# Kernel optimization log

Hardware: AMD Instinct MI355X
Metric: run time of the kernel (lower is better)

The kernel has to match this reference:

```python
import jax, jax.numpy as jnp
import numpy as np
from jax import lax

MIN_R = 0.01
RADIUS = 0.8
NSAMPLE = 32
PRED_NSAMPLE = 16
TEMPERATURE = 1.0
DIV_COEF = 10.0
GRID3 = 64  # grid_size**3, grid_size=4
EPS = 1e-5


def _ball_query(q, xyz, radius, nsample):
    """q (M,3), xyz (N,3), radius scalar or (M,). Returns idx (M,nsample) int32, empty (M,) bool.
    Mirrors stack ball_query CUDA op: first-found neighbors within radius, padded with first index."""
    N = xyz.shape[0]
    d2 = jnp.sum((q[:, None, :] - xyz[None, :, :]) ** 2, axis=-1)  # (M,N)
    r = jnp.broadcast_to(jnp.asarray(radius, d2.dtype), (q.shape[0],))[:, None]
    valid = d2 < r * r
    score = jnp.where(valid, -jnp.arange(N, dtype=jnp.int32), -(N + 1))
    vals, _ = lax.top_k(score, nsample)  # largest score == smallest valid index
    idx = -vals
    pad = idx == (N + 1)
    idx = jnp.where(pad, idx[:, :1], idx)  # pad with first found neighbor
    empty = pad[:, 0]                       # no neighbor at all
    idx = jnp.where(empty[:, None], 0, idx)
    return idx, empty


def _group(q, xyz, feats, idx, empty):
    """QueryAndGroup gather: relative xyz concat point features; zero empty queries.
    Returns (M, nsample, 3+C)."""
    g_xyz = xyz[idx] - q[:, None, :]
    g = jnp.concatenate([g_xyz, feats[idx]], axis=-1)
    return jnp.where(empty[:, None, None], jnp.zeros((), g.dtype), g)


def _mlp(x, params):
    """Shared 1x1 Conv2d + BatchNorm2d(training stats) + ReLU stack. x: (B,M,S,C)."""
    for W, g, b in params:
        x = jnp.einsum('bmsc,cd->bmsd', x, W)
        mu = x.mean(axis=(0, 1, 2))
        var = x.var(axis=(0, 1, 2))
        x = (x - mu) * lax.rsqrt(var + EPS) * g + b
        x = jax.nn.relu(x)
    return x


def setup_inputs() -> dict:
    key = jax.random.key(0)
    ks = jax.random.split(key, 16)
    B, N, C, R, Croi = 2, 8192, 32, 64, 128
    scene = jnp.array([10.0, 10.0, 4.0], jnp.float32)
    xyz = jax.random.uniform(ks[0], (B, N, 3), jnp.float32) * scene
    features = jax.random.normal(ks[1], (B, N, C), jnp.float32)
    rois = jax.random.uniform(ks[2], (B, R, GRID3, 3), jnp.float32) * scene
    roi_features = jax.random.normal(ks[3], (B, R, Croi), jnp.float32)

    def kaiming(k, fi, fo):
        return jax.random.normal(k, (fi, fo), jnp.float32) * np.float32(np.sqrt(2.0 / fi))

    return {
        'xyz': xyz, 'features': features, 'rois': rois, 'roi_features': roi_features,
        'temperature_decay': jnp.ones((1,), jnp.float32),
        # predict mlp: [32+3, 32, 32]
        'pw0': kaiming(ks[4], 35, 32), 'pg0': jnp.ones(32), 'pb0': jnp.zeros(32),
        'pw1': kaiming(ks[5], 32, 32), 'pg1': jnp.ones(32), 'pb1': jnp.zeros(32),
        # feat mlp: [32+3, 64, 64]
        'fw0': kaiming(ks[6], 35, 64), 'fg0': jnp.ones(64), 'fb0': jnp.zeros(64),
        'fw1': kaiming(ks[7], 64, 64), 'fg1': jnp.ones(64), 'fb1': jnp.zeros(64),
        # predict fc: [32*64 + 128, 1]
        'fcw': kaiming(ks[8], 2176, 1), 'fcb': jnp.zeros(1),
    }


def reference(xyz, features, rois, roi_features, temperature_decay,
              pw0, pg0, pb0, pw1, pg1, pb1,
              fw0, fg0, fb0, fw1, fg1, fb1, fcw, fcb):
    B, num_rois = rois.shape[0], rois.shape[1]
    new_xyz = rois.reshape(B, -1, 3)  # (B, M, 3), M = num_rois*grid^3

    # ---- radius-prediction branch: fixed-radius grouping + MLP + max-pool ----
    idx_p, empty_p = jax.vmap(lambda q, x: _ball_query(q, x, RADIUS, PRED_NSAMPLE))(new_xyz, xyz)
    gp = jax.vmap(_group)(new_xyz, xyz, features, idx_p, empty_p)  # (B,M,S,3+C)
    gp = _mlp(gp, [(pw0, pg0, pb0), (pw1, pg1, pb1)])
    pooled = gp.max(axis=2)                       # (B, M, Cp)
    pooled = pooled.reshape(B, num_rois, -1)      # (B, R, grid^3*Cp)
    res = jnp.concatenate([pooled, roi_features], axis=-1) @ fcw + fcb  # (B,R,1)
    r = jnp.maximum(res / DIV_COEF + RADIUS, MIN_R)
    r_pts = jnp.broadcast_to(r, (B, num_rois, GRID3)).reshape(B, -1)    # (B, M)

    # ---- deformable branch: per-query radius grouping + soft weights ----
    idx_d, empty_d = jax.vmap(lambda q, x, rr: _ball_query(q, x, rr, NSAMPLE))(new_xyz, xyz, r_pts)
    gd = jax.vmap(_group)(new_xyz, xyz, features, idx_d, empty_d)       # (B,M,S,3+C)
    dist = jnp.linalg.norm(gd[..., :3], axis=-1)                        # (B,M,S)
    w = jax.nn.sigmoid((r_pts[..., None] - dist) / (TEMPERATURE * temperature_decay[0]))
    w = jnp.where(empty_d[..., None], jnp.zeros((), w.dtype), w)
    gd = _mlp(gd, [(fw0, fg0, fb0), (fw1, fg1, fb1)])                   # (B,M,S,Cout)
    new_feats = (w[..., None] * gd).max(axis=2)                          # (B,M,Cout)

    return new_xyz.reshape(-1, 3), new_feats.reshape(-1, new_feats.shape[-1])
```

## Files before the change

kernel.cpp:

```cpp
#include <hip/hip_runtime.h>

#define NB 2
#define NPTS 8192
#define NQ 4096
#define MTOT 8192
#define SP 16
#define SD 32
#define CIN 32
#define CP 32
#define CF 64
#define NROI 128
#define RADIUS_C 0.8f
#define MIN_R_C 0.01f
#define DIV_COEF_C 10.0f

__device__ int   g_idx_p[MTOT * SP];
__device__ int   g_empty_p[MTOT];
__device__ int   g_idx_d[MTOT * SD];
__device__ int   g_empty_d[MTOT];
__device__ float g_xa[(size_t)MTOT * SD * CF];
__device__ float g_xb[(size_t)MTOT * SD * CF];
__device__ float g_psT[CF * 2048];
__device__ float g_pqT[CF * 2048];
__device__ float g_bnscale[4][CF];
__device__ float g_bnshift[4][CF];
__device__ float g_pdot[MTOT];
__device__ float g_rroi[NROI];

__global__ void copy_xyz_kernel(const float* __restrict__ rois, float* __restrict__ out) {
    int i = blockIdx.x * 256 + threadIdx.x;
    if (i < MTOT * 3) out[i] = rois[i];
}

template <int NS>
__launch_bounds__(256, 8)
__global__ void bq_kernel(const float* __restrict__ xyz, const float* __restrict__ newxyz) {
    int lane = threadIdx.x & 63;
    int q = blockIdx.x * 4 + (threadIdx.x >> 6);
    int b = q >> 12;
    const float* xb = xyz + (size_t)b * NPTS * 3;
    float qx = newxyz[q * 3 + 0], qy = newxyz[q * 3 + 1], qz = newxyz[q * 3 + 2];
    float r = (NS == SP) ? RADIUS_C : g_rroi[q >> 6];
    float r2 = r * r;
    int* idx_out   = (NS == SP) ? g_idx_p   : g_idx_d;
    int* empty_out = (NS == SP) ? g_empty_p : g_empty_d;

    int cnt = 0, first_idx = 0;
    float cx = xb[3 * lane + 0];
    float cy = xb[3 * lane + 1];
    float cz = xb[3 * lane + 2];
    for (int g = 0; g < NPTS / 64 && cnt < NS; ++g) {
        int pn = (((g + 1) & 127) << 6) + lane;
        float nx = xb[3 * pn + 0];
        float ny = xb[3 * pn + 1];
        float nz = xb[3 * pn + 2];
        float dx = qx - cx, dy = qy - cy, dz = qz - cz;
        float d2 = dx * dx + dy * dy + dz * dz;
        bool valid = d2 < r2;
        unsigned long long mask = __ballot(valid);
        if (cnt == 0 && mask) first_idx = (g << 6) + (int)__builtin_ctzll(mask);
        int pos = cnt + __popcll(mask & ((1ull << lane) - 1ull));
        if (valid && pos < NS) idx_out[q * NS + pos] = (g << 6) + lane;
        cnt += __popcll(mask);
        cx = nx; cy = ny; cz = nz;
    }
    if (cnt == 0) {
        if (lane < NS) idx_out[q * NS + lane] = 0;
        if (lane == 0) empty_out[q] = 1;
    } else {
        int filled = cnt < NS ? cnt : NS;
        if (lane >= filled && lane < NS) idx_out[q * NS + lane] = first_idx;
        if (lane == 0) empty_out[q] = 0;
    }
}


template <int NS, int CH>
__launch_bounds__(128, 4)
__global__ void mlp_passA_kernel(const float* __restrict__ xyz, const float* __restrict__ feats,
                                 const float* __restrict__ newxyz, const float* __restrict__ W0,
                                 float* __restrict__ xout) {
    constexpr int GSTR = 37;
    constexpr int SST  = CH + 2;
    __shared__ float buf[128 * GSTR];
    __shared__ float ls[128], lq[128];
    int tid = threadIdx.x;
    int rowbase = blockIdx.x * 128;
    int row = rowbase + tid;
    int q = row / NS, b = q >> 12;
    const int* idx_arr = (NS == SP) ? g_idx_p : g_idx_d;
    const int* emp_arr = (NS == SP) ? g_empty_p : g_empty_d;
    {
        float* dst = &buf[tid * GSTR];
        if (emp_arr[q]) {
#pragma unroll
            for (int c = 0; c < 35; ++c) dst[c] = 0.f;
        } else {
            int idx = idx_arr[row];
            const float* xp = xyz + (size_t)b * NPTS * 3 + idx * 3;
            dst[0] = xp[0] - newxyz[q * 3 + 0];
            dst[1] = xp[1] - newxyz[q * 3 + 1];
            dst[2] = xp[2] - newxyz[q * 3 + 2];
            const float4* fp = (const float4*)(feats + (size_t)b * NPTS * CIN + (size_t)idx * CIN);
#pragma unroll
            for (int j = 0; j < 8; ++j) {
                float4 v = fp[j];
                dst[3 + 4 * j + 0] = v.x; dst[3 + 4 * j + 1] = v.y;
                dst[3 + 4 * j + 2] = v.z; dst[3 + 4 * j + 3] = v.w;
            }
        }
    }
    float acc[CH];
#pragma unroll
    for (int ch = 0; ch < CH; ++ch) acc[ch] = 0.f;
    {
        const float* inrow = &buf[tid * GSTR];
        for (int c = 0; c < 35; ++c) {
            float h = inrow[c];
#pragma unroll
            for (int ch = 0; ch < CH; ++ch) acc[ch] = fmaf(h, W0[c * CH + ch], acc[ch]);
        }
    }
    float sum = 0.f, sq = 0.f;
#pragma unroll
    for (int p = 0; p < 2; ++p) {
        __syncthreads();
        if ((tid >> 6) == p) {
            float* srow = &buf[(tid & 63) * SST];
#pragma unroll
            for (int ch = 0; ch < CH; ++ch) srow[ch] = acc[ch];
        }
        __syncthreads();
        if (CH == 64) {
            int ch = tid & 63, rg = tid >> 6;
            for (int r = 0; r < 32; ++r) {
                float v = buf[(rg * 32 + r) * SST + ch];
                xout[(size_t)(rowbase + p * 64 + rg * 32 + r) * CH + ch] = v;
                sum += v; sq += v * v;
            }
        } else {
            int ch = tid & 31, rg = tid >> 5;
            for (int r = 0; r < 16; ++r) {
                float v = buf[(rg * 16 + r) * SST + ch];
                xout[(size_t)(rowbase + p * 64 + rg * 16 + r) * CH + ch] = v;
                sum += v; sq += v * v;
            }
        }
    }
    ls[tid] = sum; lq[tid] = sq;
    __syncthreads();
    if (CH == 64) {
        if (tid < 64) {
            g_psT[tid * 2048 + blockIdx.x] = ls[tid] + ls[64 + tid];
            g_pqT[tid * 2048 + blockIdx.x] = lq[tid] + lq[64 + tid];
        }
    } else {
        if (tid < 32) {
            g_psT[tid * 2048 + blockIdx.x] = ls[tid] + ls[32 + tid] + ls[64 + tid] + ls[96 + tid];
            g_pqT[tid * 2048 + blockIdx.x] = lq[tid] + lq[32 + tid] + lq[64 + tid] + lq[96 + tid];
        }
    }
}

template <int NS, int CH>
__launch_bounds__(128, 4)
__global__ void mlp_passB_kernel(const float* __restrict__ W1, const float* __restrict__ xin,
                                 float* __restrict__ xout, int bn0) {
    constexpr int HSTR = 33;
    constexpr int SST  = CH + 2;
    __shared__ float buf[128 * 37];
    __shared__ float ls[128], lq[128];
    int tid = threadIdx.x;
    int rowbase = blockIdx.x * 128;
    const float* sc0 = g_bnscale[bn0];
    const float* sh0 = g_bnshift[bn0];
    float acc2[CH];
#pragma unroll
    for (int ch = 0; ch < CH; ++ch) acc2[ch] = 0.f;
    const float4* src = (const float4*)xin;
#pragma unroll
    for (int hc = 0; hc < CH / 32; ++hc) {
        if (hc) __syncthreads();
#pragma unroll
        for (int k = 0; k < 8; ++k) {
            int o4 = tid + k * 128;
            int rloc = o4 >> 3, j = o4 & 7;
            int c = 4 * j, gc = hc * 32 + c;
            float4 v = src[(size_t)(rowbase + rloc) * (CH / 4) + hc * 8 + j];
            float* d = &buf[rloc * HSTR + c];
            d[0] = fmaxf(fmaf(v.x, sc0[gc + 0], sh0[gc + 0]), 0.f);
            d[1] = fmaxf(fmaf(v.y, sc0[gc + 1], sh0[gc + 1]), 0.f);
            d[2] = fmaxf(fmaf(v.z, sc0[gc + 2], sh0[gc + 2]), 0.f);
            d[3] = fmaxf(fmaf(v.w, sc0[gc + 3], sh0[gc + 3]), 0.f);
        }
        __syncthreads();
        const float* hrow = &buf[tid * HSTR];
        for (int c = 0; c < 32; ++c) {
            float h = hrow[c];
#pragma unroll
            for (int ch = 0; ch < CH; ++ch)
                acc2[ch] = fmaf(h, W1[(hc * 32 + c) * CH + ch], acc2[ch]);
        }
    }
    float sum = 0.f, sq = 0.f;
#pragma unroll
    for (int p = 0; p < 2; ++p) {
        __syncthreads();
        if ((tid >> 6) == p) {
            float* srow = &buf[(tid & 63) * SST];
#pragma unroll
            for (int ch = 0; ch < CH; ++ch) srow[ch] = acc2[ch];
        }
        __syncthreads();
        if (CH == 64) {
            int ch = tid & 63, rg = tid >> 6;
            for (int r = 0; r < 32; ++r) {
                float v = buf[(rg * 32 + r) * SST + ch];
                xout[(size_t)(rowbase + p * 64 + rg * 32 + r) * CH + ch] = v;
                sum += v; sq += v * v;
            }
        } else {
            int ch = tid & 31, rg = tid >> 5;
            for (int r = 0; r < 16; ++r) {
                float v = buf[(rg * 16 + r) * SST + ch];
                xout[(size_t)(rowbase + p * 64 + rg * 16 + r) * CH + ch] = v;
                sum += v; sq += v * v;
            }
        }
    }
    ls[tid] = sum; lq[tid] = sq;
    __syncthreads();
    if (CH == 64) {
        if (tid < 64) {
            g_psT[tid * 2048 + blockIdx.x] = ls[tid] + ls[64 + tid];
            g_pqT[tid * 2048 + blockIdx.x] = lq[tid] + lq[64 + tid];
        }
    } else {
        if (tid < 32) {
            g_psT[tid * 2048 + blockIdx.x] = ls[tid] + ls[32 + tid] + ls[64 + tid] + ls[96 + tid];
            g_pqT[tid * 2048 + blockIdx.x] = lq[tid] + lq[32 + tid] + lq[64 + tid] + lq[96 + tid];
        }
    }
}

__global__ void passC_f_kernel(const float* __restrict__ xyz, const float* __restrict__ newxyz,
                               const float* __restrict__ td, const float* __restrict__ xin,
                               float* __restrict__ out) {
    __shared__ float lw[64];
    int tid = threadIdx.x;
    int qpair = blockIdx.x * 2;
    if (tid < 64) {
        int ql = tid >> 5, s = tid & 31;
        int q = qpair + ql;
        float wv = 0.f;
        if (!g_empty_d[q]) {
            int idx = g_idx_d[q * SD + s];
            int b = q >> 12;
            float dx = xyz[(size_t)b * NPTS * 3 + idx * 3 + 0] - newxyz[q * 3 + 0];
            float dy = xyz[(size_t)b * NPTS * 3 + idx * 3 + 1] - newxyz[q * 3 + 1];
            float dz = xyz[(size_t)b * NPTS * 3 + idx * 3 + 2] - newxyz[q * 3 + 2];
            float dist = sqrtf(dx * dx + dy * dy + dz * dz);
            float rq = g_rroi[q >> 6];
            wv = 1.f / (1.f + expf(-(rq - dist) / td[0]));
        }
        lw[tid] = wv;
    }
    __syncthreads();
    int ql = tid >> 6, ch = tid & 63;
    int q = qpair + ql;
    float sc = g_bnscale[3][ch], sh = g_bnshift[3][ch];
    float m = 0.f;
    for (int s = 0; s < SD; ++s) {
        float v = xin[((size_t)q * SD + s) * CF + ch];
        m = fmaxf(m, lw[ql * 32 + s] * fmaxf(fmaf(v, sc, sh), 0.f));
    }
    out[MTOT * 3 + (size_t)q * CF + ch] = m;
}

__global__ void passC_p_kernel(const float* __restrict__ fcw, const float* __restrict__ xin) {
    int tid = threadIdx.x;
    int q = blockIdx.x * 8 + (tid >> 5);
    int ch = tid & 31;
    float sc = g_bnscale[1][ch], sh = g_bnshift[1][ch];
    float m = 0.f;
    for (int s = 0; s < SP; ++s) {
        float v = xin[(size_t)(q * SP + s) * CP + ch] * sc + sh;
        m = fmaxf(m, fmaxf(v, 0.f));
    }
    float pd = m * fcw[(q & 63) * CP + ch];
    for (int off = 16; off > 0; off >>= 1) pd += __shfl_down(pd, off, 32);
    if (ch == 0) g_pdot[q] = pd;
}

__global__ void finalize_kernel(const float* __restrict__ gamma, const float* __restrict__ beta,
                                float n, int layer, int nblocks) {
    __shared__ double l_s[256], l_q[256];
    int ch = blockIdx.x, tid = threadIdx.x;
    double s = 0, q = 0;
    for (int i = tid; i < nblocks; i += 256) { s += g_psT[ch * 2048 + i]; q += g_pqT[ch * 2048 + i]; }
    l_s[tid] = s; l_q[tid] = q; __syncthreads();
    for (int off = 128; off > 0; off >>= 1) {
        if (tid < off) { l_s[tid] += l_s[tid + off]; l_q[tid] += l_q[tid + off]; }
        __syncthreads();
    }
    if (tid == 0) {
        double mu = l_s[0] / (double)n;
        double var = l_q[0] / (double)n - mu * mu;
        if (var < 0) var = 0;
        double sc = (double)gamma[ch] / sqrt(var + 1e-5);
        g_bnscale[layer][ch] = (float)sc;
        g_bnshift[layer][ch] = (float)((double)beta[ch] - mu * sc);
    }
}

__global__ void roi_r_kernel(const float* __restrict__ roif, const float* __restrict__ fcw,
                             const float* __restrict__ fcb) {
    int tid = threadIdx.x;
    int roi = blockIdx.x * 4 + (tid >> 6);
    int lane = tid & 63;
    float acc = g_pdot[roi * 64 + lane]
              + roif[roi * 128 + lane]      * fcw[2048 + lane]
              + roif[roi * 128 + 64 + lane] * fcw[2048 + 64 + lane];
    for (int off = 32; off > 0; off >>= 1) acc += __shfl_down(acc, off, 64);
    if (lane == 0) {
        float res = acc + fcb[0];
        g_rroi[roi] = fmaxf(res / DIV_COEF_C + RADIUS_C, MIN_R_C);
    }
}

extern "C" void kernel_launch(void* const* d_in, const int* in_sizes, int n_in,
                              void* d_out, int out_size, void* d_ws, size_t ws_size,
                              hipStream_t stream) {
    const float* xyz   = (const float*)d_in[0];
    const float* feats = (const float*)d_in[1];
    const float* rois  = (const float*)d_in[2];
    const float* roif  = (const float*)d_in[3];
    const float* td    = (const float*)d_in[4];
    const float* pw0 = (const float*)d_in[5];
    const float* pg0 = (const float*)d_in[6];
    const float* pb0 = (const float*)d_in[7];
    const float* pw1 = (const float*)d_in[8];
    const float* pg1 = (const float*)d_in[9];
    const float* pb1 = (const float*)d_in[10];
    const float* fw0 = (const float*)d_in[11];
    const float* fg0 = (const float*)d_in[12];
    const float* fb0 = (const float*)d_in[13];
    const float* fw1 = (const float*)d_in[14];
    const float* fg1 = (const float*)d_in[15];
    const float* fb1 = (const float*)d_in[16];
    const float* fcw = (const float*)d_in[17];
    const float* fcb = (const float*)d_in[18];
    float* out = (float*)d_out;

    float* xa; hipGetSymbolAddress((void**)&xa, HIP_SYMBOL(g_xa));
    float* xb; hipGetSymbolAddress((void**)&xb, HIP_SYMBOL(g_xb));

    copy_xyz_kernel<<<96, 256, 0, stream>>>(rois, out);

    bq_kernel<SP><<<MTOT / 4, 256, 0, stream>>>(xyz, rois);
    mlp_passA_kernel<SP, CP><<<1024, 128, 0, stream>>>(xyz, feats, rois, pw0, xa);
    finalize_kernel<<<CP, 256, 0, stream>>>(pg0, pb0, (float)(MTOT * SP), 0, 1024);
    mlp_passB_kernel<SP, CP><<<1024, 128, 0, stream>>>(pw1, xa, xb, 0);
    finalize_kernel<<<CP, 256, 0, stream>>>(pg1, pb1, (float)(MTOT * SP), 1, 1024);
    passC_p_kernel<<<MTOT / 8, 256, 0, stream>>>(fcw, xb);
    roi_r_kernel<<<NROI / 4, 256, 0, stream>>>(roif, fcw, fcb);

    bq_kernel<SD><<<MTOT / 4, 256, 0, stream>>>(xyz, rois);
    mlp_passA_kernel<SD, CF><<<2048, 128, 0, stream>>>(xyz, feats, rois, fw0, xa);
    finalize_kernel<<<CF, 256, 0, stream>>>(fg0, fb0, (float)(MTOT * SD), 2, 2048);
    mlp_passB_kernel<SD, CF><<<2048, 128, 0, stream>>>(fw1, xa, xb, 2);
    finalize_kernel<<<CF, 256, 0, stream>>>(fg1, fb1, (float)(MTOT * SD), 3, 2048);
    passC_f_kernel<<<MTOT / 2, 128, 0, stream>>>(xyz, rois, td, xb, out);
}
```

Measured before the change: 309.6 us.

## Store deformable-branch MLP activations in fp16 and tile ball query through LDS

The deformable branch's intermediate activations (8192x32x64) are now stored as fp16 instead of fp32, with a dedicated fp16 second-layer kernel and fp16 reads in the final pooling kernel. This halves the global-memory traffic for the largest buffers. The ball query now loads 512-point tiles into shared memory cooperatively per block and exits early once all waves are full. The costs are reduced precision in the stored pre-BN activations and extra block-level syncs in the ball query.

```diff
diff --git a/kernel.cpp b/kernel.cpp
--- a/kernel.cpp
+++ b/kernel.cpp
@@ -1,4 +1,5 @@
 #include <hip/hip_runtime.h>
+#include <hip/hip_fp16.h>
 
 #define NB 2
 #define NPTS 8192
@@ -13,13 +14,14 @@
 #define RADIUS_C 0.8f
 #define MIN_R_C 0.01f
 #define DIV_COEF_C 10.0f
+#define TILE 512
 
 __device__ int   g_idx_p[MTOT * SP];
 __device__ int   g_empty_p[MTOT];
 __device__ int   g_idx_d[MTOT * SD];
 __device__ int   g_empty_d[MTOT];
-__device__ float g_xa[(size_t)MTOT * SD * CF];
-__device__ float g_xb[(size_t)MTOT * SD * CF];
+__device__ unsigned char g_xa[(size_t)MTOT * SD * CF * 2];
+__device__ unsigned char g_xb[(size_t)MTOT * SD * CF * 2];
 __device__ float g_psT[CF * 2048];
 __device__ float g_pqT[CF * 2048];
 __device__ float g_bnscale[4][CF];
@@ -35,10 +37,14 @@
 template <int NS>
 __launch_bounds__(256, 8)
 __global__ void bq_kernel(const float* __restrict__ xyz, const float* __restrict__ newxyz) {
-    int lane = threadIdx.x & 63;
-    int q = blockIdx.x * 4 + (threadIdx.x >> 6);
+    __shared__ float4 l4[TILE * 3 / 4];
+    __shared__ int s_active;
+    int tid = threadIdx.x;
+    int wave = tid >> 6, lane = tid & 63;
+    int q = blockIdx.x * 4 + wave;
     int b = q >> 12;
-    const float* xb = xyz + (size_t)b * NPTS * 3;
+    const float4* xb4 = (const float4*)(xyz + (size_t)b * NPTS * 3);
+    const float* lp = (const float*)l4;
     float qx = newxyz[q * 3 + 0], qy = newxyz[q * 3 + 1], qz = newxyz[q * 3 + 2];
     float r = (NS == SP) ? RADIUS_C : g_rroi[q >> 6];
     float r2 = r * r;
@@ -46,23 +52,29 @@
     int* empty_out = (NS == SP) ? g_empty_p : g_empty_d;
 
     int cnt = 0, first_idx = 0;
-    float cx = xb[3 * lane + 0];
-    float cy = xb[3 * lane + 1];
-    float cz = xb[3 * lane + 2];
-    for (int g = 0; g < NPTS / 64 && cnt < NS; ++g) {
-        int pn = (((g + 1) & 127) << 6) + lane;
-        float nx = xb[3 * pn + 0];
-        float ny = xb[3 * pn + 1];
-        float nz = xb[3 * pn + 2];
-        float dx = qx - cx, dy = qy - cy, dz = qz - cz;
-        float d2 = dx * dx + dy * dy + dz * dz;
-        bool valid = d2 < r2;
-        unsigned long long mask = __ballot(valid);
-        if (cnt == 0 && mask) first_idx = (g << 6) + (int)__builtin_ctzll(mask);
-        int pos = cnt + __popcll(mask & ((1ull << lane) - 1ull));
-        if (valid && pos < NS) idx_out[q * NS + pos] = (g << 6) + lane;
-        cnt += __popcll(mask);
-        cx = nx; cy = ny; cz = nz;
+    for (int t = 0; t < NPTS / TILE; ++t) {
+        l4[tid] = xb4[t * 384 + tid];
+        if (tid + 256 < 384) l4[tid + 256] = xb4[t * 384 + tid + 256];
+        if (tid == 0) s_active = 0;
+        __syncthreads();
+        if (cnt < NS) {
+            for (int s = 0; s < TILE / 64; ++s) {
+                int pl = s * 64 + lane;
+                float dx = qx - lp[3 * pl + 0];
+                float dy = qy - lp[3 * pl + 1];
+                float dz = qz - lp[3 * pl + 2];
+                bool valid = (dx * dx + dy * dy + dz * dz) < r2;
+                unsigned long long mask = __ballot(valid);
+                if (cnt == 0 && mask) first_idx = t * TILE + s * 64 + (int)__builtin_ctzll(mask);
+                int pos = cnt + __popcll(mask & ((1ull << lane) - 1ull));
+                if (valid && pos < NS) idx_out[q * NS + pos] = t * TILE + s * 64 + lane;
+                cnt += __popcll(mask);
+                if (cnt >= NS) break;
+            }
+            if (cnt < NS && lane == 0) s_active = 1;
+        }
+        __syncthreads();
+        if (!s_active) break;
     }
     if (cnt == 0) {
         if (lane < NS) idx_out[q * NS + lane] = 0;
@@ -74,12 +86,11 @@
     }
 }
 
-
-template <int NS, int CH>
+template <int NS, int CH, bool HALF>
 __launch_bounds__(128, 4)
 __global__ void mlp_passA_kernel(const float* __restrict__ xyz, const float* __restrict__ feats,
                                  const float* __restrict__ newxyz, const float* __restrict__ W0,
-                                 float* __restrict__ xout) {
+                                 void* __restrict__ xout_) {
     constexpr int GSTR = 37;
     constexpr int SST  = CH + 2;
     __shared__ float buf[128 * GSTR];
@@ -121,6 +132,8 @@
             for (int ch = 0; ch < CH; ++ch) acc[ch] = fmaf(h, W0[c * CH + ch], acc[ch]);
         }
     }
+    float* xf = (float*)xout_;
+    __half* xh = (__half*)xout_;
     float sum = 0.f, sq = 0.f;
 #pragma unroll
     for (int p = 0; p < 2; ++p) {
@@ -135,14 +148,16 @@
             int ch = tid & 63, rg = tid >> 6;
             for (int r = 0; r < 32; ++r) {
                 float v = buf[(rg * 32 + r) * SST + ch];
-                xout[(size_t)(rowbase + p * 64 + rg * 32 + r) * CH + ch] = v;
+                size_t o = (size_t)(rowbase + p * 64 + rg * 32 + r) * CH + ch;
+                if (HALF) xh[o] = __float2half_rn(v); else xf[o] = v;
                 sum += v; sq += v * v;
             }
         } else {
             int ch = tid & 31, rg = tid >> 5;
             for (int r = 0; r < 16; ++r) {
                 float v = buf[(rg * 16 + r) * SST + ch];
-                xout[(size_t)(rowbase + p * 64 + rg * 16 + r) * CH + ch] = v;
+                size_t o = (size_t)(rowbase + p * 64 + rg * 16 + r) * CH + ch;
+                if (HALF) xh[o] = __float2half_rn(v); else xf[o] = v;
                 sum += v; sq += v * v;
             }
         }
@@ -212,39 +227,84 @@
             for (int ch = 0; ch < CH; ++ch) srow[ch] = acc2[ch];
         }
         __syncthreads();
-        if (CH == 64) {
-            int ch = tid & 63, rg = tid >> 6;
-            for (int r = 0; r < 32; ++r) {
-                float v = buf[(rg * 32 + r) * SST + ch];
-                xout[(size_t)(rowbase + p * 64 + rg * 32 + r) * CH + ch] = v;
-                sum += v; sq += v * v;
-            }
-        } else {
-            int ch = tid & 31, rg = tid >> 5;
-            for (int r = 0; r < 16; ++r) {
-                float v = buf[(rg * 16 + r) * SST + ch];
-                xout[(size_t)(rowbase + p * 64 + rg * 16 + r) * CH + ch] = v;
-                sum += v; sq += v * v;
-            }
+        int ch = tid & 31, rg = tid >> 5;
+        for (int r = 0; r < 16; ++r) {
+            float v = buf[(rg * 16 + r) * SST + ch];
+            xout[(size_t)(rowbase + p * 64 + rg * 16 + r) * CH + ch] = v;
+            sum += v; sq += v * v;
         }
     }
     ls[tid] = sum; lq[tid] = sq;
     __syncthreads();
-    if (CH == 64) {
-        if (tid < 64) {
-            g_psT[tid * 2048 + blockIdx.x] = ls[tid] + ls[64 + tid];
-            g_pqT[tid * 2048 + blockIdx.x] = lq[tid] + lq[64 + tid];
-        }
-    } else {
-        if (tid < 32) {
-            g_psT[tid * 2048 + blockIdx.x] = ls[tid] + ls[32 + tid] + ls[64 + tid] + ls[96 + tid];
-            g_pqT[tid * 2048 + blockIdx.x] = lq[tid] + lq[32 + tid] + lq[64 + tid] + lq[96 + tid];
-        }
+    if (tid < 32) {
+        g_psT[tid * 2048 + blockIdx.x] = ls[tid] + ls[32 + tid] + ls[64 + tid] + ls[96 + tid];
+        g_pqT[tid * 2048 + blockIdx.x] = lq[tid] + lq[32 + tid] + lq[64 + tid] + lq[96 + tid];
+    }
+}
+
+__launch_bounds__(128, 4)
+__global__ void mlp_fB_kernel(const float* __restrict__ W1, const __half* __restrict__ xin,
+                              __half* __restrict__ xout) {
+    __shared__ float fbuf[64 * 66];
+    __shared__ float ls[128], lq[128];
+    __half* hbuf = (__half*)fbuf;
+    unsigned int* w32 = (unsigned int*)fbuf;
+    int tid = threadIdx.x;
+    int rowbase = blockIdx.x * 128;
+    {
+        const float4* src = (const float4*)xin;
+#pragma unroll
+        for (int k = 0; k < 8; ++k) {
+            int o4 = tid + k * 128;
+            int rloc = o4 >> 3, j = o4 & 7;
+            float4 v = src[(size_t)(rowbase + rloc) * 8 + j];
+            const unsigned int* s32 = (const unsigned int*)&v;
+#pragma unroll
+            for (int m = 0; m < 4; ++m) w32[rloc * 33 + 4 * j + m] = s32[m];
+        }
+    }
+    __syncthreads();
+    const float* sc0 = g_bnscale[2];
+    const float* sh0 = g_bnshift[2];
+    float acc2[CF];
+#pragma unroll
+    for (int ch = 0; ch < CF; ++ch) acc2[ch] = 0.f;
+    {
+        const __half* hrow = &hbuf[tid * 66];
+        for (int c = 0; c < 64; ++c) {
+            float h = fmaxf(fmaf(__half2float(hrow[c]), sc0[c], sh0[c]), 0.f);
+#pragma unroll
+            for (int ch = 0; ch < CF; ++ch)
+                acc2[ch] = fmaf(h, W1[c * CF + ch], acc2[ch]);
+        }
+    }
+    float sum = 0.f, sq = 0.f;
+#pragma unroll
+    for (int p = 0; p < 2; ++p) {
+        __syncthreads();
+        if ((tid >> 6) == p) {
+            float* srow = &fbuf[(tid & 63) * 66];
+#pragma unroll
+            for (int ch = 0; ch < CF; ++ch) srow[ch] = acc2[ch];
+        }
+        __syncthreads();
+        int ch = tid & 63, rg = tid >> 6;
+        for (int r = 0; r < 32; ++r) {
+            float v = fbuf[(rg * 32 + r) * 66 + ch];
+            xout[(size_t)(rowbase + p * 64 + rg * 32 + r) * CF + ch] = __float2half_rn(v);
+            sum += v; sq += v * v;
+        }
+    }
+    ls[tid] = sum; lq[tid] = sq;
+    __syncthreads();
+    if (tid < 64) {
+        g_psT[tid * 2048 + blockIdx.x] = ls[tid] + ls[64 + tid];
+        g_pqT[tid * 2048 + blockIdx.x] = lq[tid] + lq[64 + tid];
     }
 }
 
 __global__ void passC_f_kernel(const float* __restrict__ xyz, const float* __restrict__ newxyz,
-                               const float* __restrict__ td, const float* __restrict__ xin,
+                               const float* __restrict__ td, const __half* __restrict__ xin,
                                float* __restrict__ out) {
     __shared__ float lw[64];
     int tid = threadIdx.x;
@@ -271,7 +331,7 @@
     float sc = g_bnscale[3][ch], sh = g_bnshift[3][ch];
     float m = 0.f;
     for (int s = 0; s < SD; ++s) {
-        float v = xin[((size_t)q * SD + s) * CF + ch];
+        float v = __half2float(xin[((size_t)q * SD + s) * CF + ch]);
         m = fmaxf(m, lw[ql * 32 + s] * fmaxf(fmaf(v, sc, sh), 0.f));
     }
     out[MTOT * 3 + (size_t)q * CF + ch] = m;
@@ -352,23 +412,23 @@
     const float* fcb = (const float*)d_in[18];
     float* out = (float*)d_out;
 
-    float* xa; hipGetSymbolAddress((void**)&xa, HIP_SYMBOL(g_xa));
-    float* xb; hipGetSymbolAddress((void**)&xb, HIP_SYMBOL(g_xb));
+    void* xa; hipGetSymbolAddress(&xa, HIP_SYMBOL(g_xa));
+    void* xb; hipGetSymbolAddress(&xb, HIP_SYMBOL(g_xb));
 
     copy_xyz_kernel<<<96, 256, 0, stream>>>(rois, out);
 
     bq_kernel<SP><<<MTOT / 4, 256, 0, stream>>>(xyz, rois);
-    mlp_passA_kernel<SP, CP><<<1024, 128, 0, stream>>>(xyz, feats, rois, pw0, xa);
+    mlp_passA_kernel<SP, CP, false><<<1024, 128, 0, stream>>>(xyz, feats, rois, pw0, xa);
     finalize_kernel<<<CP, 256, 0, stream>>>(pg0, pb0, (float)(MTOT * SP), 0, 1024);
-    mlp_passB_kernel<SP, CP><<<1024, 128, 0, stream>>>(pw1, xa, xb, 0);
+    mlp_passB_kernel<SP, CP><<<1024, 128, 0, stream>>>(pw1, (const float*)xa, (float*)xb, 0);
     finalize_kernel<<<CP, 256, 0, stream>>>(pg1, pb1, (float)(MTOT * SP), 1, 1024);
-    passC_p_kernel<<<MTOT / 8, 256, 0, stream>>>(fcw, xb);
+    passC_p_kernel<<<MTOT / 8, 256, 0, stream>>>(fcw, (const float*)xb);
     roi_r_kernel<<<NROI / 4, 256, 0, stream>>>(roif, fcw, fcb);
 
     bq_kernel<SD><<<MTOT / 4, 256, 0, stream>>>(xyz, rois);
-    mlp_passA_kernel<SD, CF><<<2048, 128, 0, stream>>>(xyz, feats, rois, fw0, xa);
+    mlp_passA_kernel<SD, CF, true><<<2048, 128, 0, stream>>>(xyz, feats, rois, fw0, xa);
     finalize_kernel<<<CF, 256, 0, stream>>>(fg0, fb0, (float)(MTOT * SD), 2, 2048);
-    mlp_passB_kernel<SD, CF><<<2048, 128, 0, stream>>>(fw1, xa, xb, 2);
+    mlp_fB_kernel<<<2048, 128, 0, stream>>>(fw1, (const __half*)xa, (__half*)xb);
     finalize_kernel<<<CF, 256, 0, stream>>>(fg1, fb1, (float)(MTOT * SD), 3, 2048);
-    passC_f_kernel<<<MTOT / 2, 128, 0, stream>>>(xyz, rois, td, xb, out);
-}
+    passC_f_kernel<<<MTOT / 2, 128, 0, stream>>>(xyz, rois, td, (const __half*)xb, out);
+}
```

Measured after the change: 305.3 us. Within noise of the previous version (-1.4%).
